# Optimization experiments

Measured on AMD Instinct MI355X. Metric: run time of the kernel, lower is better.

The kernel has to match this reference:

```python
import jax, jax.numpy as jnp
import numpy as np

N_NODES = 100000
N_EDGES = 1250000
IN_DIM = 64
OUT_DIM = 64
N_BASES = 16
L2_EPS = 1e-12  # torch F.normalize eps


def setup_inputs() -> dict:
    key = jax.random.key(0)
    ks = jax.random.split(key, 7)
    return {
        "x": jax.random.normal(ks[0], (N_NODES, IN_DIM), dtype=jnp.float32),
        "edge_index": jax.random.randint(ks[1], (2, N_EDGES), 0, N_NODES, dtype=jnp.int64)
        if jax.config.jax_enable_x64 else jax.random.randint(ks[1], (2, N_EDGES), 0, N_NODES, dtype=jnp.int32),
        "basis_msg_wt": jax.random.normal(ks[2], (IN_DIM, OUT_DIM, N_BASES), dtype=jnp.float32) * 0.1,
        "basis_msg_bias": jax.random.normal(ks[3], (OUT_DIM, N_BASES), dtype=jnp.float32) * 0.1,
        "basis_self_wt": jax.random.normal(ks[4], (IN_DIM, OUT_DIM, N_BASES), dtype=jnp.float32) * 0.1,
        "basis_self_bias": jax.random.normal(ks[5], (OUT_DIM, N_BASES), dtype=jnp.float32) * 0.1,
        "lin_comb": jax.random.normal(ks[6], (1, N_BASES), dtype=jnp.float32) * 0.1,
    }


def reference(x, edge_index, basis_msg_wt, basis_msg_bias, basis_self_wt, basis_self_bias, lin_comb):
    c = lin_comb[0]  # [B]
    # Reconstruct relation-specific weights from bases on the fly.
    W_msg = jnp.einsum('iob,b->io', basis_msg_wt, c)      # [in, out]
    b_msg = basis_msg_bias @ c                             # [out]
    W_self = jnp.einsum('iob,b->io', basis_self_wt, c)    # [in, out]
    b_self = basis_self_bias @ c                           # [out]

    src, dst = edge_index[0], edge_index[1]
    # gather x_j, per-relation linear message
    msg = x[src] @ W_msg + b_msg                           # [E, out]
    # scatter-add aggregate to destination nodes
    agg = jax.ops.segment_sum(msg, dst, num_segments=x.shape[0])  # [N, out]
    # self transform (skip_linear=True path)
    x_self = x @ W_self + b_self                           # [N, out]
    out = agg + x_self
    # F.normalize(p=2, dim=-1): divide by max(norm, eps)
    norm = jnp.linalg.norm(out, axis=-1, keepdims=True)
    return out / jnp.maximum(norm, L2_EPS)
```

## Files before the change

### kernel.cpp

```cpp
#include <hip/hip_runtime.h>

constexpr int NN = 100000;
constexpr int NE = 1250000;
constexpr int D  = 64;
constexpr int NB = 16;

constexpr int NC = 196;
constexpr int PA_BLOCKS = 512;
constexpr int NCB = NC * PA_BLOCKS;
constexpr int NSBLK = (NCB + 255) / 256;
constexpr int EPB = (NE + PA_BLOCKS - 1) / PA_BLOCKS;

typedef __attribute__((ext_vector_type(8))) short short8v;
typedef __attribute__((ext_vector_type(4))) float float4v;

__device__ __forceinline__ unsigned short f2bf(float f) {
    unsigned u = __float_as_uint(f);
    u += 0x7fffu + ((u >> 16) & 1u);
    return (unsigned short)(u >> 16);
}

constexpr int PRE_COMBINE = 8192 + 128;
constexpr int PRE_TOTAL   = PRE_COMBINE + NN * (D / 4);
constexpr int PREP_GRID   = PA_BLOCKS + (PRE_TOTAL + 255) / 256;

__global__ void prep_kernel(const float* __restrict__ wm,
                            const float* __restrict__ bm,
                            const float* __restrict__ wsf,
                            const float* __restrict__ bsf,
                            const float* __restrict__ lc,
                            const float* __restrict__ x,
                            const int* __restrict__ ei,
                            int* __restrict__ bhist,
                            unsigned short* __restrict__ wct,
                            float* __restrict__ B,
                            unsigned short* __restrict__ xb)
{
    __shared__ int h[NC];
    const int tid = threadIdx.x;

    if (blockIdx.x < PA_BLOCKS) {
        if (tid < NC) h[tid] = 0;
        __syncthreads();
        const int begin = blockIdx.x * EPB;
        const int end = min(NE, begin + EPB);
        for (int e = begin + tid; e < end; e += 256)
            atomicAdd(&h[ei[NE + e] >> 9], 1);
        __syncthreads();
        if (tid < NC) bhist[tid * PA_BLOCKS + blockIdx.x] = h[tid];
        return;
    }

    int t = (blockIdx.x - PA_BLOCKS) * 256 + tid;
    if (t < PRE_COMBINE) {
        float c[NB];
        #pragma unroll
        for (int b = 0; b < NB; ++b) c[b] = lc[b];
        const float* p;
        if (t < 4096)      p = wm  + t * NB;
        else if (t < 8192) p = wsf + (t - 4096) * NB;
        else if (t < 8256) p = bm  + (t - 8192) * NB;
        else               p = bsf + (t - 8256) * NB;
        float s = 0.f;
        #pragma unroll
        for (int b = 0; b < NB; ++b) s += p[b] * c[b];

        if (t < 4096) {
            int i = t >> 6, o = t & 63;
            wct[o * 128 + i] = f2bf(s);
        } else if (t < 8192) {
            int u = t - 4096;
            int i = u >> 6, o = u & 63;
            wct[o * 128 + 64 + i] = f2bf(s);
        } else if (t < 8256) {
            B[t - 8192] = s;
        } else {
            B[64 + (t - 8256)] = s;
        }
    } else if (t < PRE_TOTAL) {
        int k = t - PRE_COMBINE;
        float4 v = reinterpret_cast<const float4*>(x)[k];
        ushort4 o;
        o.x = f2bf(v.x); o.y = f2bf(v.y); o.z = f2bf(v.z); o.w = f2bf(v.w);
        reinterpret_cast<ushort4*>(xb)[k] = o;
    }
}

__global__ void scan_block(int* __restrict__ data,
                           int* __restrict__ partials, int n)
{
    __shared__ int tmp[256];
    int tid = threadIdx.x;
    int i = blockIdx.x * 256 + tid;
    int c = (i < n) ? data[i] : 0;
    int v = c;
    tmp[tid] = v;
    __syncthreads();
    for (int d = 1; d < 256; d <<= 1) {
        int t = (tid >= d) ? tmp[tid - d] : 0;
        __syncthreads();
        v += t;
        tmp[tid] = v;
        __syncthreads();
    }
    if (i < n) data[i] = v - c;
    if (tid == 255) partials[blockIdx.x] = v;
}

__global__ void add_offsets(int* __restrict__ data,
                            const int* __restrict__ partials, int n)
{
    __shared__ int red[256];
    const int tid = threadIdx.x;
    int s = 0;
    for (int i = tid; i < blockIdx.x; i += 256) s += partials[i];
    red[tid] = s;
    __syncthreads();
    for (int d = 128; d; d >>= 1) {
        if (tid < d) red[tid] += red[tid + d];
        __syncthreads();
    }
    int i = blockIdx.x * 256 + tid;
    if (i < n) data[i] += red[0];
}

__global__ __launch_bounds__(256)
void passA_scatter(const int* __restrict__ ei,
                   const int* __restrict__ starts,
                   int* __restrict__ pair_buf)
{
    __shared__ int cnt[NC];
    __shared__ int base[NC];
    const int tid = threadIdx.x;
    for (int j = tid; j < NC; j += 256) {
        cnt[j] = 0;
        base[j] = starts[j * PA_BLOCKS + blockIdx.x];
    }
    __syncthreads();

    const int begin = blockIdx.x * EPB;
    const int end = min(NE, begin + EPB);
    for (int e = begin + tid; e < end; e += 256) {
        int src = ei[e];
        int dst = ei[NE + e];
        int key = dst >> 9;
        int pos = base[key] + atomicAdd(&cnt[key], 1);
        pair_buf[pos] = (src << 9) | (dst & 511);
    }
}

__global__ __launch_bounds__(512)
void passB_sort(const int* __restrict__ pair_buf,
                const int* __restrict__ starts,
                int* __restrict__ sorted_src,
                int* __restrict__ node_start,
                int* __restrict__ counts)
{
    __shared__ int tmp[512];
    __shared__ int cur[512];
    const int b = blockIdx.x;
    const int s = starts[b * PA_BLOCKS];
    const int e = (b == NC - 1) ? NE : starts[(b + 1) * PA_BLOCKS];
    const int tid = threadIdx.x;

    tmp[tid] = 0;
    __syncthreads();
    for (int i = s + tid; i < e; i += 512)
        atomicAdd(&tmp[pair_buf[i] & 511], 1);
    __syncthreads();

    int c0 = tmp[tid];
    int v = c0;
    __syncthreads();
    tmp[tid] = v;
    __syncthreads();
    for (int d = 1; d < 512; d <<= 1) {
        int t = (tid >= d) ? tmp[tid - d] : 0;
        __syncthreads();
        v += t;
        tmp[tid] = v;
        __syncthreads();
    }
    int excl = v - c0;

    const int n = (b << 9) + tid;
    if (n < NN) {
        counts[n] = c0;
        node_start[n] = s + excl;
    }
    cur[tid] = excl;
    __syncthreads();

    for (int i = s + tid; i < e; i += 512) {
        int w = pair_buf[i];
        int pos = atomicAdd(&cur[w & 511], 1);
        sorted_src[s + pos] = w >> 9;
    }
}

__global__ __launch_bounds__(256)
void gather_kernel(const unsigned int* __restrict__ xbd,
                   const int* __restrict__ sorted_src,
                   const int* __restrict__ node_start,
                   const int* __restrict__ counts,
                   unsigned int* __restrict__ aggb)
{
    const int wave = threadIdx.x >> 6;
    const int lane = threadIdx.x & 63;
    const int half = lane >> 5;
    const int dq   = lane & 31;
    const int n = blockIdx.x * 4 + wave;

    const int deg = counts[n];
    const int j0 = node_start[n];

    int idxv = 0;
    if (lane < deg) idxv = sorted_src[j0 + lane];

    float aL[8], aH[8];
    #pragma unroll
    for (int p = 0; p < 8; ++p) { aL[p] = 0.f; aH[p] = 0.f; }

    const int dmain = min(deg, 64);
    for (int jj = 0; jj < dmain; jj += 16) {
        #pragma unroll
        for (int p = 0; p < 8; ++p) {
            int pos = jj + 2 * p + half;
            int srcl = __builtin_amdgcn_ds_bpermute(pos << 2, idxv);
            unsigned int u = xbd[(((unsigned)srcl) << 5) | (unsigned)dq];
            u = (pos < dmain) ? u : 0u;
            aL[p] += __uint_as_float(u << 16);
            aH[p] += __uint_as_float(u & 0xffff0000u);
        }
    }
    for (int pos = 64 + half; pos < deg; pos += 2) {
        int srcl = sorted_src[j0 + pos];
        unsigned int u = xbd[(((unsigned)srcl) << 5) | (unsigned)dq];
        aL[0] += __uint_as_float(u << 16);
        aH[0] += __uint_as_float(u & 0xffff0000u);
    }

    float sL = ((aL[0] + aL[1]) + (aL[2] + aL[3])) + ((aL[4] + aL[5]) + (aL[6] + aL[7]));
    float sH = ((aH[0] + aH[1]) + (aH[2] + aH[3])) + ((aH[4] + aH[5]) + (aH[6] + aH[7]));

    sL += __shfl_xor(sL, 32, 64);
    sH += __shfl_xor(sH, 32, 64);

    if (half == 0) {
        unsigned pk = ((unsigned)f2bf(sH) << 16) | (unsigned)f2bf(sL);
        aggb[(((unsigned)n) << 5) | (unsigned)dq] = pk;
    }
}

constexpr int NTILES = NN / 16;
constexpr int TBLOCKS = 640;

__global__ __launch_bounds__(256)
void transform_mfma(float* __restrict__ out,
                    const unsigned short* __restrict__ aggb,
                    const unsigned short* __restrict__ xb,
                    const unsigned short* __restrict__ wct,
                    const float* __restrict__ B,
                    const int* __restrict__ counts)
{
    const int lane = threadIdx.x & 63;
    const int gq = lane >> 4;
    const int c  = lane & 15;
    const int wglob = blockIdx.x * 4 + (threadIdx.x >> 6);

    short8v wf[4][4];
    #pragma unroll
    for (int t = 0; t < 4; ++t)
        #pragma unroll
        for (int ks = 0; ks < 4; ++ks) {
            int o = t * 16 + c;
            int k0 = ks * 32 + gq * 8;
            wf[t][ks] = *reinterpret_cast<const short8v*>(wct + o * 128 + k0);
        }
    float bmv[4], bsv[4];
    #pragma unroll
    for (int t = 0; t < 4; ++t) {
        bmv[t] = B[t * 16 + c];
        bsv[t] = B[64 + t * 16 + c];
    }

    for (int tile = wglob; tile < NTILES; tile += TBLOCKS * 4) {
        const int n0 = tile * 16;
        const size_t arow = (size_t)(n0 + c) * D;

        float4v acc[4];
        #pragma unroll
        for (int t = 0; t < 4; ++t) acc[t] = (float4v){0.f, 0.f, 0.f, 0.f};

        #pragma unroll
        for (int ks = 0; ks < 2; ++ks) {
            short8v a = *reinterpret_cast<const short8v*>(aggb + arow + ks * 32 + gq * 8);
            #pragma unroll
            for (int t = 0; t < 4; ++t)
                acc[t] = __builtin_amdgcn_mfma_f32_16x16x32_bf16(a, wf[t][ks], acc[t], 0, 0, 0);
        }
        #pragma unroll
        for (int ks = 2; ks < 4; ++ks) {
            short8v a = *reinterpret_cast<const short8v*>(xb + arow + (ks - 2) * 32 + gq * 8);
            #pragma unroll
            for (int t = 0; t < 4; ++t)
                acc[t] = __builtin_amdgcn_mfma_f32_16x16x32_bf16(a, wf[t][ks], acc[t], 0, 0, 0);
        }

        float dg[4];
        #pragma unroll
        for (int q = 0; q < 4; ++q) dg[q] = (float)counts[n0 + gq * 4 + q];

        float ss[4] = {0.f, 0.f, 0.f, 0.f};
        #pragma unroll
        for (int t = 0; t < 4; ++t)
            #pragma unroll
            for (int q = 0; q < 4; ++q) {
                float v = acc[t][q] + dg[q] * bmv[t] + bsv[t];
                acc[t][q] = v;
                ss[q] += v * v;
            }
        #pragma unroll
        for (int off = 1; off <= 8; off <<= 1)
            #pragma unroll
            for (int q = 0; q < 4; ++q) ss[q] += __shfl_xor(ss[q], off, 64);

        float sc[4];
        #pragma unroll
        for (int q = 0; q < 4; ++q) sc[q] = 1.f / fmaxf(sqrtf(ss[q]), 1e-12f);

        #pragma unroll
        for (int t = 0; t < 4; ++t)
            #pragma unroll
            for (int q = 0; q < 4; ++q)
                out[(size_t)(n0 + gq * 4 + q) * D + t * 16 + c] = acc[t][q] * sc[q];
    }
}

extern "C" void kernel_launch(void* const* d_in, const int* in_sizes, int n_in,
                              void* d_out, int out_size, void* d_ws, size_t ws_size,
                              hipStream_t stream)
{
    const float* x   = (const float*)d_in[0];
    const int*   ei  = (const int*)d_in[1];
    const float* wm  = (const float*)d_in[2];
    const float* bm  = (const float*)d_in[3];
    const float* wsf = (const float*)d_in[4];
    const float* bsf = (const float*)d_in[5];
    const float* lc  = (const float*)d_in[6];

    float* out = (float*)d_out;

    float* Bv         = (float*)d_ws;
    unsigned short* wct = (unsigned short*)(Bv + 128);
    int* starts       = (int*)(wct + 8192);
    int* partials     = starts + NCB;
    int* counts       = partials + 512;
    int* node_start   = counts + NN;
    int* pair_buf     = node_start + NN;
    int* sorted_src   = pair_buf + NE;
    unsigned short* xb   = (unsigned short*)(sorted_src + NE);
    unsigned int*   aggb = (unsigned int*)(xb + (size_t)NN * D);

    prep_kernel<<<PREP_GRID, 256, 0, stream>>>(
        wm, bm, wsf, bsf, lc, x, ei, starts, wct, Bv, xb);

    scan_block<<<NSBLK, 256, 0, stream>>>(starts, partials, NCB);
    add_offsets<<<NSBLK, 256, 0, stream>>>(starts, partials, NCB);

    passA_scatter<<<PA_BLOCKS, 256, 0, stream>>>(ei, starts, pair_buf);

    passB_sort<<<NC, 512, 0, stream>>>(pair_buf, starts,
                                       sorted_src, node_start, counts);

    gather_kernel<<<NN / 4, 256, 0, stream>>>(
        (const unsigned int*)xb, sorted_src, node_start, counts, aggb);

    transform_mfma<<<TBLOCKS, 256, 0, stream>>>(
        out, (const unsigned short*)aggb, xb, wct, Bv, counts);
}
```

Measured before the change: 86.38 us.

## Fuse two-pass scan with decoupled flags and process two nodes per gather wave

Replaces the two-kernel block scan plus offset add with a single scan kernel. Each block publishes its total behind a release flag, and later blocks spin on the flags of earlier blocks to get their offset. The flags are zeroed in the prep kernel. The gather kernel now handles two destination nodes per wave and launches half as many blocks, which issues both nodes' index loads up front. The spin-wait relies on earlier blocks being scheduled first, which holds here with about 392 blocks, and it removes one launch at the cost of possible waiting.

```diff
diff --git a/kernel.cpp b/kernel.cpp
--- a/kernel.cpp
+++ b/kernel.cpp
@@ -21,7 +21,8 @@
 }
 
 constexpr int PRE_COMBINE = 8192 + 128;
-constexpr int PRE_TOTAL   = PRE_COMBINE + NN * (D / 4);
+constexpr int PRE_FLAGS   = PRE_COMBINE + NSBLK;
+constexpr int PRE_TOTAL   = PRE_FLAGS + NN * (D / 4);
 constexpr int PREP_GRID   = PA_BLOCKS + (PRE_TOTAL + 255) / 256;
 
 __global__ void prep_kernel(const float* __restrict__ wm,
@@ -34,6 +35,7 @@
                             int* __restrict__ bhist,
                             unsigned short* __restrict__ wct,
                             float* __restrict__ B,
+                            int* __restrict__ bflag,
                             unsigned short* __restrict__ xb)
 {
     __shared__ int h[NC];
@@ -77,8 +79,10 @@
         } else {
             B[64 + (t - 8256)] = s;
         }
+    } else if (t < PRE_FLAGS) {
+        bflag[t - PRE_COMBINE] = 0;
     } else if (t < PRE_TOTAL) {
-        int k = t - PRE_COMBINE;
+        int k = t - PRE_FLAGS;
         float4 v = reinterpret_cast<const float4*>(x)[k];
         ushort4 o;
         o.x = f2bf(v.x); o.y = f2bf(v.y); o.z = f2bf(v.z); o.w = f2bf(v.w);
@@ -86,12 +90,16 @@
     }
 }
 
-__global__ void scan_block(int* __restrict__ data,
-                           int* __restrict__ partials, int n)
+__global__ __launch_bounds__(256)
+void scan_fused(int* __restrict__ data,
+                int* __restrict__ bsum,
+                int* __restrict__ bflag, int n)
 {
     __shared__ int tmp[256];
-    int tid = threadIdx.x;
-    int i = blockIdx.x * 256 + tid;
+    const int b = blockIdx.x;
+    const int tid = threadIdx.x;
+    const int i = b * 256 + tid;
+
     int c = (i < n) ? data[i] : 0;
     int v = c;
     tmp[tid] = v;
@@ -103,25 +111,25 @@
         tmp[tid] = v;
         __syncthreads();
     }
-    if (i < n) data[i] = v - c;
-    if (tid == 255) partials[blockIdx.x] = v;
-}
-
-__global__ void add_offsets(int* __restrict__ data,
-                            const int* __restrict__ partials, int n)
-{
-    __shared__ int red[256];
-    const int tid = threadIdx.x;
+
+    if (tid == 255) {
+        __hip_atomic_store(&bsum[b], v, __ATOMIC_RELEASE, __HIP_MEMORY_SCOPE_AGENT);
+        __hip_atomic_store(&bflag[b], 1, __ATOMIC_RELEASE, __HIP_MEMORY_SCOPE_AGENT);
+    }
+
     int s = 0;
-    for (int i = tid; i < blockIdx.x; i += 256) s += partials[i];
-    red[tid] = s;
+    for (int k = tid; k < b; k += 256) {
+        while (__hip_atomic_load(&bflag[k], __ATOMIC_ACQUIRE, __HIP_MEMORY_SCOPE_AGENT) == 0) {}
+        s += __hip_atomic_load(&bsum[k], __ATOMIC_RELAXED, __HIP_MEMORY_SCOPE_AGENT);
+    }
+    __syncthreads();
+    tmp[tid] = s;
     __syncthreads();
     for (int d = 128; d; d >>= 1) {
-        if (tid < d) red[tid] += red[tid + d];
-        __syncthreads();
-    }
-    int i = blockIdx.x * 256 + tid;
-    if (i < n) data[i] += red[0];
+        if (tid < d) tmp[tid] += tmp[tid + d];
+        __syncthreads();
+    }
+    if (i < n) data[i] = v - c + tmp[0];
 }
 
 __global__ __launch_bounds__(256)
@@ -209,46 +217,57 @@
     const int lane = threadIdx.x & 63;
     const int half = lane >> 5;
     const int dq   = lane & 31;
-    const int n = blockIdx.x * 4 + wave;
-
-    const int deg = counts[n];
-    const int j0 = node_start[n];
-
-    int idxv = 0;
-    if (lane < deg) idxv = sorted_src[j0 + lane];
-
-    float aL[8], aH[8];
+    const int n0 = blockIdx.x * 8 + wave * 2;
+    const int n1 = n0 + 1;
+
+    const int deg0 = counts[n0];
+    const int deg1 = counts[n1];
+    const int s0 = node_start[n0];
+    const int s1 = node_start[n1];
+    int idx0 = 0, idx1 = 0;
+    if (lane < deg0) idx0 = sorted_src[s0 + lane];
+    if (lane < deg1) idx1 = sorted_src[s1 + lane];
+
     #pragma unroll
-    for (int p = 0; p < 8; ++p) { aL[p] = 0.f; aH[p] = 0.f; }
-
-    const int dmain = min(deg, 64);
-    for (int jj = 0; jj < dmain; jj += 16) {
-        #pragma unroll
-        for (int p = 0; p < 8; ++p) {
-            int pos = jj + 2 * p + half;
-            int srcl = __builtin_amdgcn_ds_bpermute(pos << 2, idxv);
+    for (int nn = 0; nn < 2; ++nn) {
+        const int deg  = nn ? deg1 : deg0;
+        const int j0   = nn ? s1 : s0;
+        const int idxv = nn ? idx1 : idx0;
+        const int n    = nn ? n1 : n0;
+
+        float aL[8], aH[8];
+        #pragma unroll
+        for (int p = 0; p < 8; ++p) { aL[p] = 0.f; aH[p] = 0.f; }
+
+        const int dmain = min(deg, 64);
+        for (int jj = 0; jj < dmain; jj += 16) {
+            #pragma unroll
+            for (int p = 0; p < 8; ++p) {
+                int pos = jj + 2 * p + half;
+                int srcl = __builtin_amdgcn_ds_bpermute(pos << 2, idxv);
+                unsigned int u = xbd[(((unsigned)srcl) << 5) | (unsigned)dq];
+                u = (pos < dmain) ? u : 0u;
+                aL[p] += __uint_as_float(u << 16);
+                aH[p] += __uint_as_float(u & 0xffff0000u);
+            }
+        }
+        for (int pos = 64 + half; pos < deg; pos += 2) {
+            int srcl = sorted_src[j0 + pos];
             unsigned int u = xbd[(((unsigned)srcl) << 5) | (unsigned)dq];
-            u = (pos < dmain) ? u : 0u;
-            aL[p] += __uint_as_float(u << 16);
-            aH[p] += __uint_as_float(u & 0xffff0000u);
-        }
-    }
-    for (int pos = 64 + half; pos < deg; pos += 2) {
-        int srcl = sorted_src[j0 + pos];
-        unsigned int u = xbd[(((unsigned)srcl) << 5) | (unsigned)dq];
-        aL[0] += __uint_as_float(u << 16);
-        aH[0] += __uint_as_float(u & 0xffff0000u);
-    }
-
-    float sL = ((aL[0] + aL[1]) + (aL[2] + aL[3])) + ((aL[4] + aL[5]) + (aL[6] + aL[7]));
-    float sH = ((aH[0] + aH[1]) + (aH[2] + aH[3])) + ((aH[4] + aH[5]) + (aH[6] + aH[7]));
-
-    sL += __shfl_xor(sL, 32, 64);
-    sH += __shfl_xor(sH, 32, 64);
-
-    if (half == 0) {
-        unsigned pk = ((unsigned)f2bf(sH) << 16) | (unsigned)f2bf(sL);
-        aggb[(((unsigned)n) << 5) | (unsigned)dq] = pk;
+            aL[0] += __uint_as_float(u << 16);
+            aH[0] += __uint_as_float(u & 0xffff0000u);
+        }
+
+        float sL = ((aL[0] + aL[1]) + (aL[2] + aL[3])) + ((aL[4] + aL[5]) + (aL[6] + aL[7]));
+        float sH = ((aH[0] + aH[1]) + (aH[2] + aH[3])) + ((aH[4] + aH[5]) + (aH[6] + aH[7]));
+
+        sL += __shfl_xor(sL, 32, 64);
+        sH += __shfl_xor(sH, 32, 64);
+
+        if (half == 0) {
+            unsigned pk = ((unsigned)f2bf(sH) << 16) | (unsigned)f2bf(sL);
+            aggb[(((unsigned)n) << 5) | (unsigned)dq] = pk;
+        }
     }
 }
 
@@ -354,8 +373,9 @@
     float* Bv         = (float*)d_ws;
     unsigned short* wct = (unsigned short*)(Bv + 128);
     int* starts       = (int*)(wct + 8192);
-    int* partials     = starts + NCB;
-    int* counts       = partials + 512;
+    int* bsum         = starts + NCB;
+    int* bflag        = bsum + 512;
+    int* counts       = bflag + 512;
     int* node_start   = counts + NN;
     int* pair_buf     = node_start + NN;
     int* sorted_src   = pair_buf + NE;
@@ -363,17 +383,16 @@
     unsigned int*   aggb = (unsigned int*)(xb + (size_t)NN * D);
 
     prep_kernel<<<PREP_GRID, 256, 0, stream>>>(
-        wm, bm, wsf, bsf, lc, x, ei, starts, wct, Bv, xb);
-
-    scan_block<<<NSBLK, 256, 0, stream>>>(starts, partials, NCB);
-    add_offsets<<<NSBLK, 256, 0, stream>>>(starts, partials, NCB);
+        wm, bm, wsf, bsf, lc, x, ei, starts, wct, Bv, bflag, xb);
+
+    scan_fused<<<NSBLK, 256, 0, stream>>>(starts, bsum, bflag, NCB);
 
     passA_scatter<<<PA_BLOCKS, 256, 0, stream>>>(ei, starts, pair_buf);
 
     passB_sort<<<NC, 512, 0, stream>>>(pair_buf, starts,
                                        sorted_src, node_start, counts);
 
-    gather_kernel<<<NN / 4, 256, 0, stream>>>(
+    gather_kernel<<<NN / 8, 256, 0, stream>>>(
         (const unsigned int*)xb, sorted_src, node_start, counts, aggb);
 
     transform_mfma<<<TBLOCKS, 256, 0, stream>>>(
```

Result: slower. 113.5 us (+31.4%).
